# Optimization experiments

Hardware: AMD Instinct MI355X
Metric: run time of the kernel (lower is better)

## Reference

```python
import jax, jax.numpy as jnp
import numpy as np

T, B, A_DIM = 64, 128, 5
N_AGENTS, N_CAP = 8, 7
OBS_D = 64
CAP_D = N_AGENTS * N_CAP  # 56
FC, HN, TGT = 128, 128, 64
D = N_CAP + 1  # transformer model dim = 8
NH, FF, NL = 4, 64, 2
EPS = 1e-6


def _ln(x, s, b):
    m = jnp.mean(x, -1, keepdims=True)
    v = jnp.mean(jnp.square(x - m), -1, keepdims=True)
    return (x - m) * jax.lax.rsqrt(v + EPS) * s + b


def _hyper(x, w1, b1, w2, b2):
    return jax.nn.relu(x @ w1 + b1) @ w2 + b2


def setup_inputs() -> dict:
    key = jax.random.key(0)
    ks = iter(jax.random.split(key, 40))

    def rn(shape, s=0.1):
        return jax.random.normal(next(ks), shape, jnp.float32) * s

    return dict(
        hidden=jnp.zeros((B, FC), jnp.float32),
        full_obs=jax.random.normal(next(ks), (T, B, OBS_D + CAP_D), jnp.float32),
        dones=jax.random.randint(next(ks), (T, B), 0, 2, jnp.int32),
        embed_w=rn((OBS_D, FC)), embed_b=jnp.zeros((FC,), jnp.float32),
        gru_wi=rn((FC, 3 * FC)), gru_wh=rn((FC, 3 * FC)), gru_bh=jnp.zeros((3 * FC,), jnp.float32),
        tWq=rn((NL, D, D), 0.3), tWk=rn((NL, D, D), 0.3), tWv=rn((NL, D, D), 0.3), tWo=rn((NL, D, D), 0.3),
        ln1_s=jnp.ones((NL, D), jnp.float32), ln1_b=jnp.zeros((NL, D), jnp.float32),
        ffw1=rn((NL, D, FF), 0.2), ffb1=jnp.zeros((NL, FF), jnp.float32),
        ffw2=rn((NL, FF, D), 0.2), ffb2=jnp.zeros((NL, D), jnp.float32),
        ln2_s=jnp.ones((NL, D), jnp.float32), ln2_b=jnp.zeros((NL, D), jnp.float32),
        hw1_1=rn((D, HN)), hb1_1=jnp.zeros((HN,), jnp.float32), hw2_1=rn((HN, FC * TGT), 0.02), hb2_1=jnp.zeros((FC * TGT,), jnp.float32),
        hw1_2=rn((D, HN)), hb1_2=jnp.zeros((HN,), jnp.float32), hw2_2=rn((HN, TGT), 0.02), hb2_2=jnp.zeros((TGT,), jnp.float32),
        hw1_3=rn((D, HN)), hb1_3=jnp.zeros((HN,), jnp.float32), hw2_3=rn((HN, TGT * A_DIM), 0.01), hb2_3=jnp.zeros((TGT * A_DIM,), jnp.float32),
        hw1_4=rn((D, HN)), hb1_4=jnp.zeros((HN,), jnp.float32), hw2_4=rn((HN, A_DIM), 0.01), hb2_4=jnp.zeros((A_DIM,), jnp.float32),
    )


def reference(hidden, full_obs, dones, embed_w, embed_b, gru_wi, gru_wh, gru_bh,
              tWq, tWk, tWv, tWo, ln1_s, ln1_b, ffw1, ffb1, ffw2, ffb2, ln2_s, ln2_b,
              hw1_1, hb1_1, hw2_1, hb2_1, hw1_2, hb1_2, hw2_2, hb2_2,
              hw1_3, hb1_3, hw2_3, hb2_3, hw1_4, hb1_4, hw2_4, hb2_4):
    obs = full_obs[:, :, :OBS_D]          # [T,B,OBS_D]
    cap = full_obs[:, :, OBS_D:]          # [T,B,CAP_D]
    emb = jax.nn.relu(obs @ embed_w + embed_b)  # [T,B,FC]
    resets = dones.astype(bool)

    # --- GRU scan over time (flax GRUCell math: input dense no bias, hidden dense with bias) ---
    def gru_step(h, xt):
        e, d = xt
        h = jnp.where(d[:, None], 0.0, h)
        gi = e @ gru_wi                   # [B, 3*FC]
        gh = h @ gru_wh + gru_bh
        ir, iz, inn = jnp.split(gi, 3, -1)
        hr, hz, hn = jnp.split(gh, 3, -1)
        r = jax.nn.sigmoid(ir + hr)
        z = jax.nn.sigmoid(iz + hz)
        n = jnp.tanh(inn + r * hn)
        hnew = (1.0 - z) * n + z * h
        return hnew, hnew

    hidden, emb_seq = jax.lax.scan(gru_step, hidden, (emb, resets))

    # --- transformer over agents dim ---
    x = cap.reshape(T * B, N_AGENTS, N_CAP)
    flag = jnp.zeros((T * B, N_AGENTS, 1), jnp.float32).at[:, 0, 0].set(1.0)
    x = jnp.concatenate([x, flag], axis=-1)   # [N, A, D]
    hd = D // NH
    scale = 1.0 / jnp.sqrt(jnp.float32(hd))
    for l in range(NL):
        q = (x @ tWq[l]).reshape(-1, N_AGENTS, NH, hd)
        k = (x @ tWk[l]).reshape(-1, N_AGENTS, NH, hd)
        v = (x @ tWv[l]).reshape(-1, N_AGENTS, NH, hd)
        att = jax.nn.softmax(jnp.einsum('nqhd,nkhd->nhqk', q, k) * scale, axis=-1)
        o = jnp.einsum('nhqk,nkhd->nqhd', att, v).reshape(-1, N_AGENTS, D) @ tWo[l]
        # original does x = norm(attn + x); x = x + dropout(x) -> doubles x
        x = 2.0 * _ln(o + x, ln1_s[l], ln1_b[l])
        ff = jax.nn.relu(x @ ffw1[l] + ffb1[l]) @ ffw2[l] + ffb2[l]
        x = 2.0 * _ln(ff + x, ln2_s[l], ln2_b[l])
    cap_repr = jnp.mean(x, axis=1).reshape(T, B, D)

    # --- hypernetworks -> per-(t,b) weights ---
    w1 = _hyper(cap_repr, hw1_1, hb1_1, hw2_1, hb2_1).reshape(T, B, FC, TGT)
    b1 = _hyper(cap_repr, hw1_2, hb1_2, hw2_2, hb2_2).reshape(T, B, 1, TGT)
    w2 = _hyper(cap_repr, hw1_3, hb1_3, hw2_3, hb2_3).reshape(T, B, TGT, A_DIM)
    b2 = _hyper(cap_repr, hw1_4, hb1_4, hw2_4, hb2_4).reshape(T, B, 1, A_DIM)

    h1 = jax.nn.relu(emb_seq[:, :, None, :] @ w1 + b1)   # [T,B,1,TGT]
    logits = (h1 @ w2 + b2).squeeze(2)                    # [T,B,A_DIM]
    return hidden, logits
```

## Files before the change

### kernel.cpp

```cpp
#include <hip/hip_runtime.h>
#include <hip/hip_bf16.h>
#include <stdint.h>

#define TT 64
#define BB 128
#define OBSD 64
#define FOBS 120
#define FC 128
#define G3 384
#define NS 8192
#define DD 8
#define FF 64
#define HN 128
#define TGT 64
#define ADIM 5

typedef __attribute__((ext_vector_type(8))) short bf16x8;
typedef __attribute__((ext_vector_type(4))) float f32x4;

__device__ __forceinline__ float sigmoidf_(float x) { return 1.0f / (1.0f + __expf(-x)); }
__device__ __forceinline__ float tanhf_(float x) {
    float e = __expf(-2.0f * fabsf(x));
    float r = (1.0f - e) / (1.0f + e);
    return copysignf(r, x);
}
__device__ __forceinline__ unsigned short f2bf_rne(float x) {
    unsigned u = __float_as_uint(x);
    return (unsigned short)((u + 0x7fffu + ((u >> 16) & 1u)) >> 16);
}

__global__ __launch_bounds__(256) void k_embed(
    const float* __restrict__ fobs, const float* __restrict__ We,
    const float* __restrict__ be, float* __restrict__ emb)
{
    __shared__ float obs_t[64][68];
    __shared__ float W_t[64][128];
    int tid = threadIdx.x;
    int s0 = blockIdx.x * 64;
    {
        int rl = tid >> 4, e4 = tid & 15;
#pragma unroll
        for (int rr = 0; rr < 4; ++rr) {
            int r = rl + rr * 16;
            float4 v = *(const float4*)&fobs[(size_t)(s0 + r) * FOBS + e4 * 4];
            *(float4*)&obs_t[r][e4 * 4] = v;
        }
    }
#pragma unroll
    for (int i = 0; i < 8; ++i) {
        int idx = tid + i * 256;
        int e = idx >> 5, c4 = idx & 31;
        float4 v = *(const float4*)&We[(size_t)e * 128 + c4 * 4];
        *(float4*)&W_t[e][c4 * 4] = v;
    }
    __syncthreads();
    int c = tid & 127, half = tid >> 7;
    float acc[32];
    float bc = be[c];
#pragma unroll
    for (int k = 0; k < 32; ++k) acc[k] = bc;
#pragma unroll
    for (int e4 = 0; e4 < 16; ++e4) {
        float w0 = W_t[4 * e4 + 0][c], w1 = W_t[4 * e4 + 1][c];
        float w2 = W_t[4 * e4 + 2][c], w3 = W_t[4 * e4 + 3][c];
#pragma unroll
        for (int k = 0; k < 32; ++k) {
            float4 ov = *(const float4*)&obs_t[half * 32 + k][e4 * 4];
            acc[k] += ov.x * w0 + ov.y * w1 + ov.z * w2 + ov.w * w3;
        }
    }
#pragma unroll
    for (int k = 0; k < 32; ++k)
        emb[(size_t)(s0 + half * 32 + k) * FC + c] = fmaxf(acc[k], 0.0f);
}

__global__ __launch_bounds__(256) void k_gi(
    const float* __restrict__ emb, const float* __restrict__ Wi, float* __restrict__ gi)
{
    __shared__ float e_t[64][132];
    __shared__ float w_t[128 * 64];
    int tid = threadIdx.x;
    int st = blockIdx.x / 6, gt = blockIdx.x % 6;
    int s0 = st * 64, g0 = gt * 64;
#pragma unroll
    for (int i = 0; i < 8; ++i) {
        int idx = tid + i * 256;
        int r = idx >> 5, c4 = idx & 31;
        float4 v = *(const float4*)&emb[(size_t)(s0 + r) * FC + c4 * 4];
        *(float4*)&e_t[r][c4 * 4] = v;
    }
#pragma unroll
    for (int i = 0; i < 8; ++i) {
        int idx = tid + i * 256;
        int r = idx >> 4, g4 = idx & 15;
        float4 v = *(const float4*)&Wi[(size_t)r * G3 + g0 + g4 * 4];
        *(float4*)&w_t[r * 64 + g4 * 4] = v;
    }
    __syncthreads();
    int sb4 = (tid >> 4) * 4, ob4 = (tid & 15) * 4;
    float acc[4][4];
#pragma unroll
    for (int a = 0; a < 4; ++a)
#pragma unroll
        for (int b = 0; b < 4; ++b) acc[a][b] = 0.0f;
    for (int c4 = 0; c4 < 32; ++c4) {
        float4 e4[4], w4[4];
#pragma unroll
        for (int si = 0; si < 4; ++si) e4[si] = *(const float4*)&e_t[sb4 + si][c4 * 4];
#pragma unroll
        for (int cc = 0; cc < 4; ++cc) w4[cc] = *(const float4*)&w_t[(c4 * 4 + cc) * 64 + ob4];
#pragma unroll
        for (int si = 0; si < 4; ++si) {
            const float* ep = (const float*)&e4[si];
#pragma unroll
            for (int cc = 0; cc < 4; ++cc) {
                float ev = ep[cc];
                const float* wp = (const float*)&w4[cc];
                acc[si][0] += ev * wp[0];
                acc[si][1] += ev * wp[1];
                acc[si][2] += ev * wp[2];
                acc[si][3] += ev * wp[3];
            }
        }
    }
#pragma unroll
    for (int si = 0; si < 4; ++si) {
        float4 sv;
        sv.x = acc[si][0]; sv.y = acc[si][1]; sv.z = acc[si][2]; sv.w = acc[si][3];
        *(float4*)&gi[(size_t)(s0 + sb4 + si) * G3 + g0 + ob4] = sv;
    }
}

__global__ __launch_bounds__(256) void k_prepW(
    const float* __restrict__ W, unsigned short* __restrict__ W_swz)
{
    int fid = blockIdx.x * 256 + threadIdx.x;
    int lane = fid & 63;
    int nt = (fid >> 6) & 3;
    int ks = (fid >> 8) & 3;
    int j  = fid >> 10;
    int col = nt * 16 + (lane & 15);
    int kbase = ks * 32 + ((lane >> 4) * 8);
    const float* src = W + ((size_t)j * 128 + kbase) * 64 + col;
    unsigned short o[8];
#pragma unroll
    for (int i = 0; i < 8; ++i) o[i] = f2bf_rne(src[(size_t)i * 64]);
    *(uint4*)&W_swz[(size_t)fid * 8] = *(const uint4*)o;
}

__global__ __launch_bounds__(512, 2) void k_gru(
    const float* __restrict__ gi, const float* __restrict__ Wh, const float* __restrict__ bh,
    const int* __restrict__ dones, const float* __restrict__ h0,
    float* __restrict__ emb_seq, unsigned short* __restrict__ embb,
    float* __restrict__ hid_out)
{
    __shared__ float h_lds[2][144];
    int b = blockIdx.x, tid = threadIdx.x;
    int c = tid >> 2, q = tid & 3;
    int posc = (c >> 5) * 36 + (c & 31);

    float W[96];
#pragma unroll
    for (int g = 0; g < 3; ++g)
#pragma unroll
        for (int i = 0; i < 32; ++i)
            W[g * 32 + i] = Wh[(size_t)(q * 32 + i) * G3 + g * 128 + c];
    float bq0 = bh[c], bq1 = bh[128 + c], bq2 = bh[256 + c];

    if (tid < 128) h_lds[0][(tid >> 5) * 36 + (tid & 31)] = h0[(size_t)b * FC + tid];

    const float* g0p = gi + ((size_t)0 * BB + b) * G3;
    const float* g1p = gi + ((size_t)1 * BB + b) * G3;
    float gc0 = g0p[c], gc1 = g0p[128 + c], gc2 = g0p[256 + c];
    float n10 = g1p[c], n11 = g1p[128 + c], n12 = g1p[256 + c];
    int dval = dones[b];
    int dn1 = dones[BB + b];
    __syncthreads();

    int cur = 0;
    for (int t = 0; t < TT; ++t) {
        int t2 = (t + 2 < TT) ? t + 2 : TT - 1;
        const float* gp2 = gi + ((size_t)t2 * BB + b) * G3;
        float p0 = gp2[c], p1 = gp2[128 + c], p2 = gp2[256 + c];
        int pd = dones[t2 * BB + b];

        float d0 = 0.f, d1 = 0.f, d2 = 0.f;
        const float* hb = &h_lds[cur][q * 36];
#pragma unroll
        for (int i4 = 0; i4 < 8; ++i4) {
            float4 h4 = *(const float4*)&hb[i4 * 4];
            const float* hp = (const float*)&h4;
#pragma unroll
            for (int e = 0; e < 4; ++e) {
                int i = i4 * 4 + e;
                d0 += W[i] * hp[e];
                d1 += W[32 + i] * hp[e];
                d2 += W[64 + i] * hp[e];
            }
        }
        d0 += __shfl_xor(d0, 1, 64); d0 += __shfl_xor(d0, 2, 64);
        d1 += __shfl_xor(d1, 1, 64); d1 += __shfl_xor(d1, 2, 64);
        d2 += __shfl_xor(d2, 1, 64); d2 += __shfl_xor(d2, 2, 64);

        float hs = dval ? 0.0f : 1.0f;
        float hold = h_lds[cur][posc];
        float r = sigmoidf_(gc0 + d0 * hs + bq0);
        float z = sigmoidf_(gc1 + d1 * hs + bq1);
        float n = tanhf_(gc2 + r * (d2 * hs + bq2));
        float hnew = (1.0f - z) * n + z * (hs * hold);

        if (q == 0) {
            h_lds[cur ^ 1][posc] = hnew;
            emb_seq[((size_t)t * BB + b) * FC + c] = hnew;
            embb[((size_t)t * BB + b) * FC + c] = f2bf_rne(hnew);
        }
        gc0 = n10; gc1 = n11; gc2 = n12;
        n10 = p0;  n11 = p1;  n12 = p2;
        dval = dn1; dn1 = pd;
        __syncthreads();
        cur ^= 1;
    }
    if (tid < 128) hid_out[(size_t)b * FC + tid] = h_lds[cur][(tid >> 5) * 36 + (tid & 31)];
}

__global__ __launch_bounds__(256) void k_attn(
    const float* __restrict__ fobs,
    const float* __restrict__ tWq, const float* __restrict__ tWk,
    const float* __restrict__ tWv, const float* __restrict__ tWo,
    const float* __restrict__ ln1s, const float* __restrict__ ln1b,
    const float* __restrict__ ffw1, const float* __restrict__ ffb1,
    const float* __restrict__ ffw2, const float* __restrict__ ffb2,
    const float* __restrict__ ln2s, const float* __restrict__ ln2b,
    float* __restrict__ cap_repr)
{
    __shared__ float wq[2][8][8], wk[2][8][8], wv[2][8][8], wo[2][8][8];
    __shared__ float l1s[2][8], l1b[2][8], l2s[2][8], l2b[2][8];
    __shared__ float f1[2][8][64], fb1[2][64];
    __shared__ float f2[2][64][8], fb2w[2][8];
    __shared__ float k_l[32][8][9], v_l[32][8][9];
    int tid = threadIdx.x;
    for (int i = tid; i < 128; i += 256) {
        ((float*)wq)[i] = tWq[i]; ((float*)wk)[i] = tWk[i];
        ((float*)wv)[i] = tWv[i]; ((float*)wo)[i] = tWo[i];
        ((float*)fb1)[i] = ffb1[i];
    }
    if (tid < 16) {
        ((float*)l1s)[tid] = ln1s[tid]; ((float*)l1b)[tid] = ln1b[tid];
        ((float*)l2s)[tid] = ln2s[tid]; ((float*)l2b)[tid] = ln2b[tid];
        ((float*)fb2w)[tid] = ffb2[tid];
    }
    for (int i = tid; i < 1024; i += 256) { ((float*)f1)[i] = ffw1[i]; ((float*)f2)[i] = ffw2[i]; }
    int sl = tid >> 3, a = tid & 7;
    int s = blockIdx.x * 32 + sl;
    float x[8];
#pragma unroll
    for (int i = 0; i < 7; ++i) x[i] = fobs[(size_t)s * FOBS + OBSD + a * 7 + i];
    x[7] = (a == 0) ? 1.0f : 0.0f;
    __syncthreads();
    for (int l = 0; l < 2; ++l) {
        float q[8], k[8], v[8];
#pragma unroll
        for (int d = 0; d < 8; ++d) { q[d] = 0.f; k[d] = 0.f; v[d] = 0.f; }
#pragma unroll
        for (int e = 0; e < 8; ++e) {
            float xe = x[e];
#pragma unroll
            for (int d = 0; d < 8; ++d) {
                q[d] += xe * wq[l][e][d];
                k[d] += xe * wk[l][e][d];
                v[d] += xe * wv[l][e][d];
            }
        }
#pragma unroll
        for (int d = 0; d < 8; ++d) { k_l[sl][a][d] = k[d]; v_l[sl][a][d] = v[d]; }
        __syncthreads();
        float o[8];
#pragma unroll
        for (int h = 0; h < 4; ++h) {
            float sc[8]; float mx = -1e30f;
#pragma unroll
            for (int ka = 0; ka < 8; ++ka) {
                float sv = (q[2 * h] * k_l[sl][ka][2 * h] + q[2 * h + 1] * k_l[sl][ka][2 * h + 1])
                           * 0.70710678118654752f;
                sc[ka] = sv; mx = fmaxf(mx, sv);
            }
            float ssum = 0.f;
#pragma unroll
            for (int ka = 0; ka < 8; ++ka) { sc[ka] = __expf(sc[ka] - mx); ssum += sc[ka]; }
            float inv = 1.0f / ssum;
            float o0 = 0.f, o1 = 0.f;
#pragma unroll
            for (int ka = 0; ka < 8; ++ka) {
                float at = sc[ka] * inv;
                o0 += at * v_l[sl][ka][2 * h];
                o1 += at * v_l[sl][ka][2 * h + 1];
            }
            o[2 * h] = o0; o[2 * h + 1] = o1;
        }
        float y[8];
#pragma unroll
        for (int e = 0; e < 8; ++e) y[e] = x[e];
#pragma unroll
        for (int d = 0; d < 8; ++d) {
            float od = o[d];
#pragma unroll
            for (int e = 0; e < 8; ++e) y[e] += od * wo[l][d][e];
        }
        {
            float m = 0.f;
#pragma unroll
            for (int e = 0; e < 8; ++e) m += y[e];
            m *= 0.125f;
            float vv = 0.f;
#pragma unroll
            for (int e = 0; e < 8; ++e) { float dd = y[e] - m; vv += dd * dd; }
            vv *= 0.125f;
            float rs = rsqrtf(vv + 1e-6f);
#pragma unroll
            for (int e = 0; e < 8; ++e)
                x[e] = 2.0f * ((y[e] - m) * rs * l1s[l][e] + l1b[l][e]);
        }
        float t1[64];
#pragma unroll
        for (int f = 0; f < 64; ++f) t1[f] = 0.f;
#pragma unroll
        for (int e = 0; e < 8; ++e) {
            float xe = x[e];
#pragma unroll
            for (int f = 0; f < 64; ++f) t1[f] += xe * f1[l][e][f];
        }
        float y2[8];
#pragma unroll
        for (int e = 0; e < 8; ++e) y2[e] = x[e] + fb2w[l][e];
#pragma unroll
        for (int f = 0; f < 64; ++f) {
            float tf = fmaxf(t1[f] + fb1[l][f], 0.0f);
#pragma unroll
            for (int e = 0; e < 8; ++e) y2[e] += tf * f2[l][f][e];
        }
        {
            float m = 0.f;
#pragma unroll
            for (int e = 0; e < 8; ++e) m += y2[e];
            m *= 0.125f;
            float vv = 0.f;
#pragma unroll
            for (int e = 0; e < 8; ++e) { float dd = y2[e] - m; vv += dd * dd; }
            vv *= 0.125f;
            float rs = rsqrtf(vv + 1e-6f);
#pragma unroll
            for (int e = 0; e < 8; ++e)
                x[e] = 2.0f * ((y2[e] - m) * rs * l2s[l][e] + l2b[l][e]);
        }
        __syncthreads();
    }
#pragma unroll
    for (int e = 0; e < 8; ++e) {
        float xv = x[e];
        xv += __shfl_xor(xv, 1, 8);
        xv += __shfl_xor(xv, 2, 8);
        xv += __shfl_xor(xv, 4, 8);
        if (a == 0) cap_repr[(size_t)s * 8 + e] = xv * 0.125f;
    }
}

__global__ __launch_bounds__(256) void k_hyper(
    const float* __restrict__ cap_repr, const float* __restrict__ emb_seq,
    const float* __restrict__ hw1_1, const float* __restrict__ hb1_1,
    const float* __restrict__ hw1_2, const float* __restrict__ hb1_2,
    const float* __restrict__ hw1_3, const float* __restrict__ hb1_3,
    const float* __restrict__ hw1_4, const float* __restrict__ hb1_4,
    const float* __restrict__ hb2_1,
    const float* __restrict__ hw2_2, const float* __restrict__ hb2_2,
    const float* __restrict__ hw2_3, const float* __restrict__ hb2_3,
    const float* __restrict__ hw2_4, const float* __restrict__ hb2_4,
    float* __restrict__ hh1g, float* __restrict__ b1eff,
    float* __restrict__ w2h, float* __restrict__ b2h)
{
    __shared__ float cr[16][8];
    __shared__ float hh[4][16][132];
    __shared__ float es[16][132];
    int tid = threadIdx.x;
    int s0 = blockIdx.x * 16;
    if (tid < 128) ((float*)cr)[tid] = cap_repr[(size_t)s0 * 8 + tid];
#pragma unroll
    for (int i = 0; i < 2; ++i) {
        int idx = tid + i * 256;
        int r = idx >> 5, c4 = idx & 31;
        float4 v = *(const float4*)&emb_seq[(size_t)(s0 + r) * FC + c4 * 4];
        *(float4*)&es[r][c4 * 4] = v;
    }
    __syncthreads();
#pragma unroll
    for (int it = 0; it < 32; ++it) {
        int idx = tid + it * 256;
        int u = idx & 127;
        int sn = (idx >> 7) & 15;
        int n = idx >> 11;
        const float* w = (n == 0) ? hw1_1 : ((n == 1) ? hw1_2 : ((n == 2) ? hw1_3 : hw1_4));
        const float* bb = (n == 0) ? hb1_1 : ((n == 1) ? hb1_2 : ((n == 2) ? hb1_3 : hb1_4));
        float acc = bb[u];
#pragma unroll
        for (int e = 0; e < 8; ++e) acc += cr[sn][e] * w[e * 128 + u];
        acc = fmaxf(acc, 0.0f);
        hh[n][sn][u] = acc;
        if (n == 0) hh1g[(size_t)(s0 + sn) * 128 + u] = acc;
    }
    __syncthreads();
#pragma unroll
    for (int it = 0; it < 4; ++it) {
        int idx = tid + it * 256;
        int o = idx & 63, sn = idx >> 6;
        float acc = hb2_2[o];
        for (int j = 0; j < 128; ++j) acc += hh[1][sn][j] * hw2_2[j * 64 + o];
        for (int c = 0; c < 128; ++c) acc += es[sn][c] * hb2_1[c * 64 + o];
        b1eff[(size_t)(s0 + sn) * 64 + o] = acc;
    }
    for (int it = 0; it < 2; ++it) {
        int oa = tid + it * 256;
        if (oa < 320) {
            float acc[16];
#pragma unroll
            for (int sn = 0; sn < 16; ++sn) acc[sn] = 0.f;
            for (int j = 0; j < 128; ++j) {
                float w = hw2_3[j * 320 + oa];
#pragma unroll
                for (int sn = 0; sn < 16; ++sn) acc[sn] += hh[2][sn][j] * w;
            }
            float bb = hb2_3[oa];
#pragma unroll
            for (int sn = 0; sn < 16; ++sn) w2h[(size_t)(s0 + sn) * 320 + oa] = acc[sn] + bb;
        }
    }
    if (tid < 80) {
        int aa = tid % 5, sn = tid / 5;
        float acc = hb2_4[aa];
        for (int j = 0; j < 128; ++j) acc += hh[3][sn][j] * hw2_4[j * 5 + aa];
        b2h[(size_t)(s0 + sn) * 5 + aa] = acc;
    }
}

__global__ __launch_bounds__(256) void k_bigmm_mfma(
    const unsigned short* __restrict__ embb, const float* __restrict__ hh1g,
    const unsigned short* __restrict__ W_swz, float* __restrict__ partials)
{
    __shared__ uint4 w_lds[1024];
    __shared__ float hh1_lds[64][33];
    int tid = threadIdx.x;
    int w = tid >> 6, lane = tid & 63;
    int mt = blockIdx.x >> 2, ksp = blockIdx.x & 3;
    int s0 = mt * 64, j0 = ksp * 32;

#pragma unroll
    for (int it = 0; it < 8; ++it) {
        int idx = tid + it * 256;
        int r = idx >> 5, jj = idx & 31;
        hh1_lds[r][jj] = hh1g[(size_t)(s0 + r) * 128 + j0 + jj];
    }

    bf16x8 emb_r[2][4];
    int rbase = s0 + (w >> 1) * 32 + (lane & 15);
    int cbase = (lane >> 4) * 8;
#pragma unroll
    for (int rt = 0; rt < 2; ++rt)
#pragma unroll
        for (int ks = 0; ks < 4; ++ks)
            emb_r[rt][ks] = *(const bf16x8*)&embb[(size_t)(rbase + rt * 16) * 128 + ks * 32 + cbase];

    const uint4* Wg = (const uint4*)W_swz;
    uint4 wreg[4];
#pragma unroll
    for (int q = 0; q < 4; ++q) wreg[q] = Wg[(size_t)j0 * 1024 + q * 256 + tid];

    int nt0 = (w & 1) * 2;
    f32x4 acc[2][2];
#pragma unroll
    for (int a = 0; a < 2; ++a)
#pragma unroll
        for (int b = 0; b < 2; ++b) acc[a][b] = (f32x4){0.f, 0.f, 0.f, 0.f};

    int rl0 = (w >> 1) * 32 + 4 * (lane >> 4);
    for (int jj = 0; jj < 32; ++jj) {
        __syncthreads();
#pragma unroll
        for (int q = 0; q < 4; ++q) w_lds[q * 256 + tid] = wreg[q];
        if (jj < 31) {
#pragma unroll
            for (int q = 0; q < 4; ++q) wreg[q] = Wg[(size_t)(j0 + jj + 1) * 1024 + q * 256 + tid];
        }
        __syncthreads();
        f32x4 P00 = (f32x4){0.f, 0.f, 0.f, 0.f};
        f32x4 P01 = (f32x4){0.f, 0.f, 0.f, 0.f};
        f32x4 P10 = (f32x4){0.f, 0.f, 0.f, 0.f};
        f32x4 P11 = (f32x4){0.f, 0.f, 0.f, 0.f};
#pragma unroll
        for (int ks = 0; ks < 4; ++ks) {
            bf16x8 b0 = *(const bf16x8*)&w_lds[(ks * 4 + nt0) * 64 + lane];
            bf16x8 b1 = *(const bf16x8*)&w_lds[(ks * 4 + nt0 + 1) * 64 + lane];
            P00 = __builtin_amdgcn_mfma_f32_16x16x32_bf16(emb_r[0][ks], b0, P00, 0, 0, 0);
            P01 = __builtin_amdgcn_mfma_f32_16x16x32_bf16(emb_r[0][ks], b1, P01, 0, 0, 0);
            P10 = __builtin_amdgcn_mfma_f32_16x16x32_bf16(emb_r[1][ks], b0, P10, 0, 0, 0);
            P11 = __builtin_amdgcn_mfma_f32_16x16x32_bf16(emb_r[1][ks], b1, P11, 0, 0, 0);
        }
#pragma unroll
        for (int r = 0; r < 4; ++r) {
            float h0 = hh1_lds[rl0 + r][jj];
            float h1 = hh1_lds[rl0 + 16 + r][jj];
            acc[0][0][r] += h0 * P00[r];
            acc[0][1][r] += h0 * P01[r];
            acc[1][0][r] += h1 * P10[r];
            acc[1][1][r] += h1 * P11[r];
        }
    }
    float* pb = partials + (size_t)ksp * (NS * 64);
#pragma unroll
    for (int rt = 0; rt < 2; ++rt) {
#pragma unroll
        for (int n = 0; n < 2; ++n) {
            int colg = (w & 1) * 32 + n * 16 + (lane & 15);
#pragma unroll
            for (int r = 0; r < 4; ++r) {
                int rowg = s0 + (w >> 1) * 32 + rt * 16 + 4 * (lane >> 4) + r;
                pb[(size_t)rowg * 64 + colg] = acc[rt][n][r];
            }
        }
    }
}

__global__ __launch_bounds__(256) void k_final(
    const float* __restrict__ partials, const float* __restrict__ b1eff,
    const float* __restrict__ w2h, const float* __restrict__ b2h, float* __restrict__ out)
{
    int tid = threadIdx.x;
    int wv = tid >> 6, lane = tid & 63;
    int s = blockIdx.x * 4 + wv;
    float h1 = b1eff[(size_t)s * 64 + lane];
#pragma unroll
    for (int ks = 0; ks < 4; ++ks) h1 += partials[(size_t)ks * (NS * 64) + (size_t)s * 64 + lane];
    h1 = fmaxf(h1, 0.0f);
    float lg[5];
#pragma unroll
    for (int aa = 0; aa < 5; ++aa) lg[aa] = h1 * w2h[(size_t)s * 320 + lane * 5 + aa];
#pragma unroll
    for (int off = 32; off >= 1; off >>= 1) {
#pragma unroll
        for (int aa = 0; aa < 5; ++aa) lg[aa] += __shfl_xor(lg[aa], off, 64);
    }
    if (lane == 0) {
#pragma unroll
        for (int aa = 0; aa < 5; ++aa)
            out[16384 + (size_t)s * 5 + aa] = lg[aa] + b2h[(size_t)s * 5 + aa];
    }
}

extern "C" void kernel_launch(void* const* d_in, const int* in_sizes, int n_in,
                              void* d_out, int out_size, void* d_ws, size_t ws_size,
                              hipStream_t stream)
{
    (void)in_sizes; (void)n_in; (void)out_size; (void)ws_size;
    const float* hidden  = (const float*)d_in[0];
    const float* fobs    = (const float*)d_in[1];
    const int*   dones   = (const int*)d_in[2];
    const float* embed_w = (const float*)d_in[3];
    const float* embed_b = (const float*)d_in[4];
    const float* gru_wi  = (const float*)d_in[5];
    const float* gru_wh  = (const float*)d_in[6];
    const float* gru_bh  = (const float*)d_in[7];
    const float* tWq  = (const float*)d_in[8];
    const float* tWk  = (const float*)d_in[9];
    const float* tWv  = (const float*)d_in[10];
    const float* tWo  = (const float*)d_in[11];
    const float* ln1s = (const float*)d_in[12];
    const float* ln1b = (const float*)d_in[13];
    const float* ffw1 = (const float*)d_in[14];
    const float* ffb1 = (const float*)d_in[15];
    const float* ffw2 = (const float*)d_in[16];
    const float* ffb2 = (const float*)d_in[17];
    const float* ln2s = (const float*)d_in[18];
    const float* ln2b = (const float*)d_in[19];
    const float* hw1_1 = (const float*)d_in[20]; const float* hb1_1 = (const float*)d_in[21];
    const float* hw2_1 = (const float*)d_in[22]; const float* hb2_1 = (const float*)d_in[23];
    const float* hw1_2 = (const float*)d_in[24]; const float* hb1_2 = (const float*)d_in[25];
    const float* hw2_2 = (const float*)d_in[26]; const float* hb2_2 = (const float*)d_in[27];
    const float* hw1_3 = (const float*)d_in[28]; const float* hb1_3 = (const float*)d_in[29];
    const float* hw2_3 = (const float*)d_in[30]; const float* hb2_3 = (const float*)d_in[31];
    const float* hw1_4 = (const float*)d_in[32]; const float* hb1_4 = (const float*)d_in[33];
    const float* hw2_4 = (const float*)d_in[34]; const float* hb2_4 = (const float*)d_in[35];
    float* out = (float*)d_out;
    float* ws  = (float*)d_ws;

    float* gi      = ws;
    float* parts   = ws;
    float* emb     = gi      + 3145728;
    unsigned short* W_swz    = (unsigned short*)emb;
    unsigned short* emb_bf16 = (unsigned short*)(emb + 524288);
    float* emb_seq = emb     + 1048576;
    float* cap_rep = emb_seq + 1048576;
    float* hh1g    = cap_rep + 65536;
    float* b1eff_  = hh1g    + 1048576;
    float* w2hb    = b1eff_  + 524288;
    float* b2hb    = w2hb    + 2621440;

    k_embed<<<128, 256, 0, stream>>>(fobs, embed_w, embed_b, emb);
    k_gi<<<768, 256, 0, stream>>>(emb, gru_wi, gi);
    k_prepW<<<512, 256, 0, stream>>>(hw2_1, W_swz);
    k_gru<<<128, 512, 0, stream>>>(gi, gru_wh, gru_bh, dones, hidden, emb_seq, emb_bf16, out);
    k_attn<<<256, 256, 0, stream>>>(fobs, tWq, tWk, tWv, tWo, ln1s, ln1b,
                                    ffw1, ffb1, ffw2, ffb2, ln2s, ln2b, cap_rep);
    k_hyper<<<512, 256, 0, stream>>>(cap_rep, emb_seq,
                                     hw1_1, hb1_1, hw1_2, hb1_2, hw1_3, hb1_3, hw1_4, hb1_4,
                                     hb2_1, hw2_2, hb2_2, hw2_3, hb2_3, hw2_4, hb2_4,
                                     hh1g, b1eff_, w2hb, b2hb);
    k_bigmm_mfma<<<512, 256, 0, stream>>>(emb_bf16, hh1g, W_swz, parts);
    k_final<<<2048, 256, 0, stream>>>(parts, b1eff_, w2hb, b2hb, out);
}
```

Before: 381.4 us.

## Give each wave its own N-tile and stream weights from global registers without LDS

The swizzled weight layout is reordered so that each output column tile (nt) is contiguous across j. In the big hypernetwork matmul, each of the 4 waves now owns one 16-column tile for all 64 rows and reads its B fragments straight from global memory into registers, with a 4-deep prefetch ring. The per-j LDS staging and the two barriers per iteration are removed, and hh1 is stored transposed so it can be read with float4 loads. In exchange each wave holds 16 A fragments and 16 B fragments in registers, which raises register pressure, and loses the sharing of each weight fragment between two waves through LDS.

```diff
diff --git a/kernel.cpp b/kernel.cpp
--- a/kernel.cpp
+++ b/kernel.cpp
@@ -136,16 +136,17 @@
 {
     int fid = blockIdx.x * 256 + threadIdx.x;
     int lane = fid & 63;
-    int nt = (fid >> 6) & 3;
-    int ks = (fid >> 8) & 3;
-    int j  = fid >> 10;
+    int ks = (fid >> 6) & 3;
+    int j  = (fid >> 8) & 127;
+    int nt = (fid >> 15);
     int col = nt * 16 + (lane & 15);
     int kbase = ks * 32 + ((lane >> 4) * 8);
     const float* src = W + ((size_t)j * 128 + kbase) * 64 + col;
     unsigned short o[8];
 #pragma unroll
     for (int i = 0; i < 8; ++i) o[i] = f2bf_rne(src[(size_t)i * 64]);
-    *(uint4*)&W_swz[(size_t)fid * 8] = *(const uint4*)o;
+    size_t slot = ((size_t)((nt * 128 + j) * 4 + ks)) * 64 + lane;
+    *(uint4*)&W_swz[slot * 8] = *(const uint4*)o;
 }
 
 __global__ __launch_bounds__(512, 2) void k_gru(
@@ -444,10 +445,9 @@
     const unsigned short* __restrict__ embb, const float* __restrict__ hh1g,
     const unsigned short* __restrict__ W_swz, float* __restrict__ partials)
 {
-    __shared__ uint4 w_lds[1024];
-    __shared__ float hh1_lds[64][33];
+    __shared__ float hh1T[32][68];
     int tid = threadIdx.x;
-    int w = tid >> 6, lane = tid & 63;
+    int nt = tid >> 6, lane = tid & 63;
     int mt = blockIdx.x >> 2, ksp = blockIdx.x & 3;
     int s0 = mt * 64, j0 = ksp * 32;
 
@@ -455,74 +455,68 @@
     for (int it = 0; it < 8; ++it) {
         int idx = tid + it * 256;
         int r = idx >> 5, jj = idx & 31;
-        hh1_lds[r][jj] = hh1g[(size_t)(s0 + r) * 128 + j0 + jj];
-    }
-
-    bf16x8 emb_r[2][4];
-    int rbase = s0 + (w >> 1) * 32 + (lane & 15);
+        hh1T[jj][r] = hh1g[(size_t)(s0 + r) * 128 + j0 + jj];
+    }
+
+    bf16x8 emb_r[4][4];
+    int rrow = lane & 15;
     int cbase = (lane >> 4) * 8;
 #pragma unroll
-    for (int rt = 0; rt < 2; ++rt)
+    for (int rt = 0; rt < 4; ++rt)
 #pragma unroll
         for (int ks = 0; ks < 4; ++ks)
-            emb_r[rt][ks] = *(const bf16x8*)&embb[(size_t)(rbase + rt * 16) * 128 + ks * 32 + cbase];
-
-    const uint4* Wg = (const uint4*)W_swz;
-    uint4 wreg[4];
-#pragma unroll
-    for (int q = 0; q < 4; ++q) wreg[q] = Wg[(size_t)j0 * 1024 + q * 256 + tid];
-
-    int nt0 = (w & 1) * 2;
-    f32x4 acc[2][2];
-#pragma unroll
-    for (int a = 0; a < 2; ++a)
-#pragma unroll
-        for (int b = 0; b < 2; ++b) acc[a][b] = (f32x4){0.f, 0.f, 0.f, 0.f};
-
-    int rl0 = (w >> 1) * 32 + 4 * (lane >> 4);
-    for (int jj = 0; jj < 32; ++jj) {
-        __syncthreads();
-#pragma unroll
-        for (int q = 0; q < 4; ++q) w_lds[q * 256 + tid] = wreg[q];
-        if (jj < 31) {
-#pragma unroll
-            for (int q = 0; q < 4; ++q) wreg[q] = Wg[(size_t)(j0 + jj + 1) * 1024 + q * 256 + tid];
-        }
-        __syncthreads();
-        f32x4 P00 = (f32x4){0.f, 0.f, 0.f, 0.f};
-        f32x4 P01 = (f32x4){0.f, 0.f, 0.f, 0.f};
-        f32x4 P10 = (f32x4){0.f, 0.f, 0.f, 0.f};
-        f32x4 P11 = (f32x4){0.f, 0.f, 0.f, 0.f};
-#pragma unroll
-        for (int ks = 0; ks < 4; ++ks) {
-            bf16x8 b0 = *(const bf16x8*)&w_lds[(ks * 4 + nt0) * 64 + lane];
-            bf16x8 b1 = *(const bf16x8*)&w_lds[(ks * 4 + nt0 + 1) * 64 + lane];
-            P00 = __builtin_amdgcn_mfma_f32_16x16x32_bf16(emb_r[0][ks], b0, P00, 0, 0, 0);
-            P01 = __builtin_amdgcn_mfma_f32_16x16x32_bf16(emb_r[0][ks], b1, P01, 0, 0, 0);
-            P10 = __builtin_amdgcn_mfma_f32_16x16x32_bf16(emb_r[1][ks], b0, P10, 0, 0, 0);
-            P11 = __builtin_amdgcn_mfma_f32_16x16x32_bf16(emb_r[1][ks], b1, P11, 0, 0, 0);
-        }
+            emb_r[rt][ks] = *(const bf16x8*)&embb[(size_t)(s0 + rt * 16 + rrow) * 128 + ks * 32 + cbase];
+
+    const bf16x8* Wg = (const bf16x8*)W_swz + ((size_t)(nt * 128 + j0) * 4) * 64 + lane;
+    bf16x8 bf[4][4];
+#pragma unroll
+    for (int s = 0; s < 4; ++s)
+#pragma unroll
+        for (int q = 0; q < 4; ++q) bf[s][q] = Wg[(size_t)s * 256 + q * 64];
+
+    f32x4 acc[4];
+#pragma unroll
+    for (int rt = 0; rt < 4; ++rt) acc[rt] = (f32x4){0.f, 0.f, 0.f, 0.f};
+
+    int hrow = 4 * (lane >> 4);
+    __syncthreads();
+
+    for (int jj = 0; jj < 32; jj += 4) {
+#pragma unroll
+        for (int s = 0; s < 4; ++s) {
+            int j = jj + s;
+            f32x4 P[4];
+#pragma unroll
+            for (int rt = 0; rt < 4; ++rt) P[rt] = (f32x4){0.f, 0.f, 0.f, 0.f};
+#pragma unroll
+            for (int ks = 0; ks < 4; ++ks) {
+                bf16x8 b = bf[s][ks];
+#pragma unroll
+                for (int rt = 0; rt < 4; ++rt)
+                    P[rt] = __builtin_amdgcn_mfma_f32_16x16x32_bf16(emb_r[rt][ks], b, P[rt], 0, 0, 0);
+            }
+            if (j + 4 < 32) {
+#pragma unroll
+                for (int q = 0; q < 4; ++q) bf[s][q] = Wg[(size_t)(j + 4) * 256 + q * 64];
+            }
+            const float* hp = &hh1T[j][hrow];
+#pragma unroll
+            for (int rt = 0; rt < 4; ++rt) {
+                float4 h4 = *(const float4*)&hp[rt * 16];
+                const float* hv = (const float*)&h4;
+#pragma unroll
+                for (int r = 0; r < 4; ++r) acc[rt][r] += hv[r] * P[rt][r];
+            }
+        }
+    }
+    float* pb = partials + (size_t)ksp * (NS * 64);
+    int colg = nt * 16 + (lane & 15);
+#pragma unroll
+    for (int rt = 0; rt < 4; ++rt) {
 #pragma unroll
         for (int r = 0; r < 4; ++r) {
-            float h0 = hh1_lds[rl0 + r][jj];
-            float h1 = hh1_lds[rl0 + 16 + r][jj];
-            acc[0][0][r] += h0 * P00[r];
-            acc[0][1][r] += h0 * P01[r];
-            acc[1][0][r] += h1 * P10[r];
-            acc[1][1][r] += h1 * P11[r];
-        }
-    }
-    float* pb = partials + (size_t)ksp * (NS * 64);
-#pragma unroll
-    for (int rt = 0; rt < 2; ++rt) {
-#pragma unroll
-        for (int n = 0; n < 2; ++n) {
-            int colg = (w & 1) * 32 + n * 16 + (lane & 15);
-#pragma unroll
-            for (int r = 0; r < 4; ++r) {
-                int rowg = s0 + (w >> 1) * 32 + rt * 16 + 4 * (lane >> 4) + r;
-                pb[(size_t)rowg * 64 + colg] = acc[rt][n][r];
-            }
+            int rowg = s0 + rt * 16 + hrow + r;
+            pb[(size_t)rowg * 64 + colg] = acc[rt][r];
         }
     }
 }
```

After: 463.4 us. 21.5% more time.
